# Kernel optimization log

Measured on AMD Instinct MI355X. Metric: run time of the kernel, lower is better.

Reference implementation:

```python
import jax, jax.numpy as jnp
import numpy as np

B, N, DIM, H = 2, 2048, 1024, 16
HD = DIM // H
SCALE = HD ** -0.5


def setup_inputs() -> dict:
    key = jax.random.key(0)
    ks = jax.random.split(key, 11)
    std = DIM ** -0.5
    inp = {
        'q': jax.random.normal(ks[0], (B, N, DIM), jnp.float32),
        'k': jax.random.normal(ks[1], (B, N, DIM), jnp.float32),
        'v': jax.random.normal(ks[2], (B, N, DIM), jnp.float32),
        # causal mask, broadcast over batch and heads; mask==0 -> masked out
        'mask': jnp.tril(jnp.ones((N, N), jnp.int32))[None, None],
        'Wq': jax.random.normal(ks[3], (DIM, DIM), jnp.float32) * std,
        'bq': jnp.zeros((DIM,), jnp.float32),
        'Wk': jax.random.normal(ks[4], (DIM, DIM), jnp.float32) * std,
        'bk': jnp.zeros((DIM,), jnp.float32),
        'Wv': jax.random.normal(ks[5], (DIM, DIM), jnp.float32) * std,
        'bv': jnp.zeros((DIM,), jnp.float32),
        'Wo': jax.random.normal(ks[6], (DIM, DIM), jnp.float32) * std,
        'bo': jnp.zeros((DIM,), jnp.float32),
    }
    return inp


def _split_heads(x):  # [b, n, dim] -> [b, h, n, c]
    b, n, _ = x.shape
    return x.reshape(b, n, H, HD).transpose(0, 2, 1, 3)


def reference(q, k, v, mask, Wq, bq, Wk, bk, Wv, bv, Wo, bo):
    qh = _split_heads(q @ Wq.T + bq)                      # [b,h,nq,c]
    kh = _split_heads(k @ Wk.T + bk)                      # [b,h,nk,c]
    vh = _split_heads(v @ Wv.T + bv)                      # [b,h,nk,c]
    attn = jnp.einsum('bhqc,bhkc->bhqk', qh, kh) * SCALE  # [b,h,nq,nk]
    attn = jnp.where(mask == 0, -jnp.inf, attn)
    attn = jax.nn.softmax(attn, axis=-1)
    out = jnp.einsum('bhqk,bhkc->bhqc', attn, vh)          # [b,h,nq,c]
    b, h, n, c = out.shape
    out = out.transpose(0, 2, 1, 3).reshape(b, n, h * c)   # [b,nq,dim]
    return out @ Wo.T + bo
```

## Files before the change

### kernel.cpp

```cpp
#include <hip/hip_runtime.h>

#define NN 2048
#define DIMD 1024
#define HH 16
#define HDD 64
#define SC2 0.1803368801111244f

typedef __attribute__((ext_vector_type(8))) short bf16x8;
typedef __attribute__((ext_vector_type(4))) float f32x4;
typedef __attribute__((ext_vector_type(4))) _Float16 f16x4;
typedef __attribute__((ext_vector_type(2))) __fp16 hf16x2;
typedef unsigned short ushort_t;
typedef unsigned int uint_t;

#define MFMA32(a, b, c) __builtin_amdgcn_mfma_f32_16x16x32_bf16((a), (b), (c), 0, 0, 0)
#define MFMA16H(a, b, c) __builtin_amdgcn_mfma_f32_16x16x16f16((a), (b), (c), 0, 0, 0)

__device__ __forceinline__ ushort_t f2bf(float f) {
    union { float f; uint_t u; } v; v.f = f;
    uint_t u = v.u;
    return (ushort_t)((u + 0x7FFFu + ((u >> 16) & 1u)) >> 16);
}
__device__ __forceinline__ void gl_lds16(const ushort_t* g, ushort_t* l) {
    __builtin_amdgcn_global_load_lds(
        (const __attribute__((address_space(1))) void*)g,
        (__attribute__((address_space(3))) void*)l, 16, 0, 0);
}

__global__ __launch_bounds__(256) void convert_k(
    const float* __restrict__ q, const float* __restrict__ k, const float* __restrict__ v,
    const float* __restrict__ wq, const float* __restrict__ wk,
    const float* __restrict__ wv, const float* __restrict__ wo,
    ushort_t* __restrict__ Abf, ushort_t* __restrict__ Wbf) {
    size_t gid = (size_t)blockIdx.x * 256 + threadIdx.x;
    size_t e = gid * 8;
    const float* src; ushort_t* dst;
    float sc = 1.f;
    if (e < 12582912) {
        int i = (int)(e >> 22);
        src = (i == 0 ? q : (i == 1 ? k : v)) + (e & 4194303);
        dst = Abf + e;
    } else {
        size_t e2 = e - 12582912;
        int i = (int)(e2 >> 20);
        src = (i == 0 ? wq : (i == 1 ? wk : (i == 2 ? wv : wo))) + (e2 & 1048575);
        dst = Wbf + e2;
        if (i == 0) sc = SC2;
    }
    float4 x = ((const float4*)src)[0], y = ((const float4*)src)[1];
    union { uint4 u; ushort_t s[8]; } pk;
    pk.s[0] = f2bf(x.x * sc); pk.s[1] = f2bf(x.y * sc); pk.s[2] = f2bf(x.z * sc); pk.s[3] = f2bf(x.w * sc);
    pk.s[4] = f2bf(y.x * sc); pk.s[5] = f2bf(y.y * sc); pk.s[6] = f2bf(y.z * sc); pk.s[7] = f2bf(y.w * sc);
    *(uint4*)dst = pk.u;
}

template<int MODE, int TM>
__global__ __launch_bounds__(256, TM == 128 ? 3 : 5) void gemm_k(
    const ushort_t* __restrict__ Abase, const ushort_t* __restrict__ Wbase,
    const float* __restrict__ b0p, const float* __restrict__ b1p, const float* __restrict__ b2p,
    ushort_t* __restrict__ d0, ushort_t* __restrict__ d1, ushort_t* __restrict__ d2,
    float* __restrict__ fout) {
    const int K = 1024;
    constexpr int MT = TM / 32;
    __shared__ ushort_t As[2][TM * 32];
    __shared__ ushort_t Bs[2][128 * 32];
    int z = (MODE == 0) ? blockIdx.z : 0;
    const ushort_t* A = Abase + (size_t)z * 4096 * 1024;
    const ushort_t* W = Wbase + (size_t)z * 1024 * 1024;
    const float* bias = (MODE == 0) ? (z == 0 ? b0p : (z == 1 ? b1p : b2p)) : b0p;
    int tid = threadIdx.x;
    int m0 = blockIdx.x * TM, n0 = blockIdx.y * 128;
    int lane = tid & 63, wave = tid >> 6;
    int quad = lane >> 4, l15 = lane & 15;
    int wm = (wave >> 1) * (TM / 2), wn = (wave & 1) * 64;

    f32x4 acc[MT][4];
    for (int i = 0; i < MT; i++)
        for (int j = 0; j < 4; j++)
            acc[i][j] = (f32x4){0.f, 0.f, 0.f, 0.f};

    int rA = tid >> 2, cA = tid & 3;
    int gA = cA ^ ((rA >> 1) & 3);

    auto stage = [&](int buf, int k0) {
        gl_lds16(A + (size_t)(m0 + rA) * K + k0 + gA * 8, &As[buf][tid * 8]);
        if (TM == 128)
            gl_lds16(A + (size_t)(m0 + rA + 64) * K + k0 + gA * 8, &As[buf][(tid + 256) * 8]);
        gl_lds16(W + (size_t)(n0 + rA) * K + k0 + gA * 8, &Bs[buf][tid * 8]);
        gl_lds16(W + (size_t)(n0 + rA + 64) * K + k0 + gA * 8, &Bs[buf][(tid + 256) * 8]);
    };
    stage(0, 0);

    int fc = (quad ^ ((l15 >> 1) & 3)) * 8;

    for (int it = 0; it < 32; it++) {
        int cur = it & 1;
        __syncthreads();
        if (it < 31) stage(1 - cur, (it + 1) * 32);
        bf16x8 a[MT], b[4];
        for (int mt = 0; mt < MT; mt++)
            a[mt] = *(const bf16x8*)&As[cur][(wm + mt * 16 + l15) * 32 + fc];
        for (int nt = 0; nt < 4; nt++)
            b[nt] = *(const bf16x8*)&Bs[cur][(wn + nt * 16 + l15) * 32 + fc];
        for (int mt = 0; mt < MT; mt++)
            for (int nt = 0; nt < 4; nt++)
                acc[mt][nt] = MFMA32(a[mt], b[nt], acc[mt][nt]);
    }
    if (MODE == 0 && z == 2) {
        for (int nt = 0; nt < 4; nt++) {
            int n = n0 + wn + nt * 16 + l15;
            float bv = bias[n];
            int h = n >> 6, c = n & 63;
            for (int mt = 0; mt < MT; mt++) {
                int mb = m0 + wm + mt * 16 + quad * 4;
                int b = mb >> 11, ns = mb & 2047;
                union { uint2 u2; _Float16 hh[4]; } pkv;
                pkv.hh[0] = (_Float16)(acc[mt][nt][0] + bv);
                pkv.hh[1] = (_Float16)(acc[mt][nt][1] + bv);
                pkv.hh[2] = (_Float16)(acc[mt][nt][2] + bv);
                pkv.hh[3] = (_Float16)(acc[mt][nt][3] + bv);
                *(uint2*)&d2[(((size_t)(b * HH + h)) * HDD + c) * NN + ns] = pkv.u2;
            }
        }
    } else {
        for (int nt = 0; nt < 4; nt++) {
            int n = n0 + wn + nt * 16 + l15;
            float bv = bias[n];
            if (MODE == 0 && z == 0) bv *= SC2;
            for (int mt = 0; mt < MT; mt++)
                for (int r = 0; r < 4; r++) {
                    int m = m0 + wm + mt * 16 + quad * 4 + r;
                    float val = acc[mt][nt][r] + bv;
                    if (MODE == 0) {
                        int b = m >> 11, ns = m & 2047;
                        int h = n >> 6, c = n & 63;
                        ushort_t* dst = (z == 0) ? d0 : d1;
                        dst[(((size_t)(b * HH + h)) * NN + ns) * HDD + c] = f2bf(val);
                    } else {
                        fout[(size_t)m * DIMD + n] = val;
                    }
                }
        }
    }
}

__global__ __launch_bounds__(256, 2) void attn9(const ushort_t* __restrict__ Qh,
                                                const ushort_t* __restrict__ Kh,
                                                const ushort_t* __restrict__ VtG,
                                                ushort_t* __restrict__ aout) {
    __shared__ ushort_t Kb[2][2][64 * 64];
    __shared__ ushort_t Vb[2][2][64 * 64];
    int tid = threadIdx.x, lane = tid & 63, w = tid >> 6;
    int quad = lane >> 4, l15 = lane & 15;
    int bh = blockIdx.y;
    int qa = blockIdx.x;
    int qc = 31 - qa;
    const ushort_t* Qp = Qh + (size_t)bh * NN * HDD;
    const ushort_t* Kp = Kh + (size_t)bh * NN * HDD;
    const ushort_t* Vp = VtG + (size_t)bh * HDD * NN;
    int ra = qa * 64 + w * 16;
    int rc = qc * 64 + w * 16;

    bf16x8 aqa[2], aqc[2];
    for (int kk = 0; kk < 2; kk++) {
        aqa[kk] = *(const bf16x8*)&Qp[(size_t)(ra + l15) * HDD + kk * 32 + quad * 8];
        aqc[kk] = *(const bf16x8*)&Qp[(size_t)(rc + l15) * HDD + kk * 32 + quad * 8];
    }
    asm volatile("" :: "v"(aqa[0]), "v"(aqa[1]), "v"(aqc[0]), "v"(aqc[1]));

    f32x4 oa[4], oc[4], ola, olc;
    for (int ct = 0; ct < 4; ct++) {
        oa[ct] = (f32x4){0.f, 0.f, 0.f, 0.f};
        oc[ct] = (f32x4){0.f, 0.f, 0.f, 0.f};
    }
    ola = (f32x4){0.f, 0.f, 0.f, 0.f};
    olc = (f32x4){0.f, 0.f, 0.f, 0.f};
    const f16x4 vone = {(_Float16)1.f, (_Float16)1.f, (_Float16)1.f, (_Float16)1.f};

    int sr0 = tid >> 3, scg = tid & 7;
    int ssc = scg ^ (sr0 & 7);
    int key = l15 & 7;
    int c0 = (quad ^ key) * 8;
    int c1 = ((4 + quad) ^ key) * 8;

    auto stageK = [&](int s, int kt) {
        for (int h = 0; h < 2; h++) {
            int kr = kt * 128 + h * 64;
            gl_lds16(Kp + (size_t)(kr + sr0) * HDD + ssc * 8,      &Kb[s][h][(0 * 256 + w * 64) * 8]);
            gl_lds16(Kp + (size_t)(kr + sr0 + 32) * HDD + ssc * 8, &Kb[s][h][(1 * 256 + w * 64) * 8]);
            gl_lds16(Vp + (size_t)sr0 * NN + kr + ssc * 8,         &Vb[s][h][(0 * 256 + w * 64) * 8]);
            gl_lds16(Vp + (size_t)(sr0 + 32) * NN + kr + ssc * 8,  &Vb[s][h][(1 * 256 + w * 64) * 8]);
        }
    };

    int kbmax = qc >> 1;
    int kam   = qa >> 1;
    stageK(0, 0);

    auto doHalf = [&](const bf16x8 (&aq)[2], f32x4 (&o)[4], f32x4& ol,
                      int rowb, const ushort_t* Kl, const ushort_t* Vl,
                      int kvb, bool diag) {
        bf16x8 kf0[4], kf1[4];
        for (int nt = 0; nt < 4; nt++) {
            kf0[nt] = *(const bf16x8*)&Kl[(nt * 16 + l15) * 64 + c0];
            kf1[nt] = *(const bf16x8*)&Kl[(nt * 16 + l15) * 64 + c1];
        }
        f32x4 s[4];
        __builtin_amdgcn_s_setprio(1);
        for (int nt = 0; nt < 4; nt++) {
            f32x4 z = (f32x4){0.f, 0.f, 0.f, 0.f};
            z = MFMA32(kf0[nt], aq[0], z);
            s[nt] = MFMA32(kf1[nt], aq[1], z);
        }
        __builtin_amdgcn_s_setprio(0);
        f16x4 ap[4];
        if (diag) {
            for (int nt = 0; nt < 4; nt++) {
                float pp[4];
                for (int r = 0; r < 4; r++) {
                    int kv = kvb + nt * 16 + quad * 4 + r;
                    pp[r] = (kv <= rowb + l15) ? __builtin_amdgcn_exp2f(s[nt][r]) : 0.f;
                }
                union { hf16x2 h2[2]; f16x4 h4; } u;
                u.h2[0] = __builtin_amdgcn_cvt_pkrtz(pp[0], pp[1]);
                u.h2[1] = __builtin_amdgcn_cvt_pkrtz(pp[2], pp[3]);
                ap[nt] = u.h4;
            }
        } else {
            for (int nt = 0; nt < 4; nt++) {
                union { hf16x2 h2[2]; f16x4 h4; } u;
                u.h2[0] = __builtin_amdgcn_cvt_pkrtz(__builtin_amdgcn_exp2f(s[nt][0]),
                                                     __builtin_amdgcn_exp2f(s[nt][1]));
                u.h2[1] = __builtin_amdgcn_cvt_pkrtz(__builtin_amdgcn_exp2f(s[nt][2]),
                                                     __builtin_amdgcn_exp2f(s[nt][3]));
                ap[nt] = u.h4;
            }
        }
        f16x4 vf[4][4];
        for (int ct = 0; ct < 4; ct++)
            for (int nt = 0; nt < 4; nt++)
                vf[ct][nt] = *(const f16x4*)&Vl[(ct * 16 + l15) * 64 +
                                ((2 * nt + (quad >> 1)) ^ key) * 8 + (quad & 1) * 4];
        __builtin_amdgcn_s_setprio(1);
        for (int nt = 0; nt < 4; nt++)
            ol = MFMA16H(ap[nt], vone, ol);
        for (int ct = 0; ct < 4; ct++)
            for (int nt = 0; nt < 4; nt++)
                o[ct] = MFMA16H(ap[nt], vf[ct][nt], o[ct]);
        __builtin_amdgcn_s_setprio(0);
    };

    int cur = 0;
    for (int kb2 = 0; kb2 <= kbmax; kb2++) {
        __syncthreads();
        if (kb2 < kbmax) stageK(cur ^ 1, kb2 + 1);
        bool dc = (kb2 == kbmax);
        for (int h = 0; h < 2; h++)
            doHalf(aqc, oc, olc, rc, &Kb[cur][h][0], &Vb[cur][h][0],
                   kb2 * 128 + h * 64, dc);
        if (kb2 <= kam) {
            bool da = (kb2 == kam);
            for (int h = 0; h < 2; h++)
                doHalf(aqa, oa, ola, ra, &Kb[cur][h][0], &Vb[cur][h][0],
                       kb2 * 128 + h * 64, da);
        }
        cur ^= 1;
    }

    int b = bh >> 4, h = bh & 15;
    for (int r = 0; r < 4; r++) {
        float ila = 1.f / ola[r];
        float ilc = 1.f / olc[r];
        for (int ct = 0; ct < 4; ct++) {
            int c = ct * 16 + l15;
            int qqa = ra + quad * 4 + r;
            int qqc = rc + quad * 4 + r;
            aout[((size_t)(b * NN + qqa)) * DIMD + h * HDD + c] = f2bf(oa[ct][r] * ila);
            aout[((size_t)(b * NN + qqc)) * DIMD + h * HDD + c] = f2bf(oc[ct][r] * ilc);
        }
    }
}

extern "C" void kernel_launch(void* const* d_in, const int* in_sizes, int n_in,
                              void* d_out, int out_size, void* d_ws, size_t ws_size,
                              hipStream_t stream) {
    const float* q  = (const float*)d_in[0];
    const float* k  = (const float*)d_in[1];
    const float* v  = (const float*)d_in[2];
    const float* Wq = (const float*)d_in[4];
    const float* bq = (const float*)d_in[5];
    const float* Wk = (const float*)d_in[6];
    const float* bk = (const float*)d_in[7];
    const float* Wv = (const float*)d_in[8];
    const float* bv = (const float*)d_in[9];
    const float* Wo = (const float*)d_in[10];
    const float* bo = (const float*)d_in[11];
    float* out = (float*)d_out;

    char* ws = (char*)d_ws;
    ushort_t* Abf  = (ushort_t*)(ws);
    ushort_t* Wbf  = (ushort_t*)(ws + (24ull << 20));
    ushort_t* Qh   = (ushort_t*)(ws + (32ull << 20));
    ushort_t* Kh   = (ushort_t*)(ws + (40ull << 20));
    ushort_t* VtG  = (ushort_t*)(ws + (48ull << 20));
    ushort_t* AObf = (ushort_t*)(ws + (56ull << 20));

    hipLaunchKernelGGL(convert_k, dim3(8192), dim3(256), 0, stream,
                       q, k, v, Wq, Wk, Wv, Wo, Abf, Wbf);
    hipLaunchKernelGGL((gemm_k<0, 128>), dim3(32, 8, 3), dim3(256), 0, stream,
                       Abf, Wbf, bq, bk, bv, Qh, Kh, VtG, (float*)nullptr);
    hipLaunchKernelGGL(attn9, dim3(16, 32), dim3(256), 0, stream, Qh, Kh, VtG, AObf);
    hipLaunchKernelGGL((gemm_k<1, 64>), dim3(64, 8, 1), dim3(256), 0, stream,
                       AObf, Wbf + 3ull * 1024 * 1024, bo, nullptr, nullptr,
                       nullptr, nullptr, nullptr, out);
}
```

Before: 221.0 us.

## Fuse fp32-to-bf16 activation conversion into the QKV projection GEMM

The separate conversion of q, k and v to bf16 is removed. A new QKV GEMM kernel reads the fp32 activations directly into registers, converts them with packed bf16 convert instructions, and writes them into swizzled LDS, while the weights are still staged through global_load_lds. This removes a full write and re-read of the 24MB bf16 activation copy. In exchange the GEMM reads twice as many bytes for A and does the conversion work inside its main loop, which may lengthen each loop iteration.

```diff
diff --git a/kernel.cpp b/kernel.cpp
--- a/kernel.cpp
+++ b/kernel.cpp
@@ -27,31 +27,121 @@
         (__attribute__((address_space(3))) void*)l, 16, 0, 0);
 }
 
-__global__ __launch_bounds__(256) void convert_k(
-    const float* __restrict__ q, const float* __restrict__ k, const float* __restrict__ v,
+__global__ __launch_bounds__(256) void convert_w(
     const float* __restrict__ wq, const float* __restrict__ wk,
     const float* __restrict__ wv, const float* __restrict__ wo,
-    ushort_t* __restrict__ Abf, ushort_t* __restrict__ Wbf) {
-    size_t gid = (size_t)blockIdx.x * 256 + threadIdx.x;
-    size_t e = gid * 8;
-    const float* src; ushort_t* dst;
-    float sc = 1.f;
-    if (e < 12582912) {
-        int i = (int)(e >> 22);
-        src = (i == 0 ? q : (i == 1 ? k : v)) + (e & 4194303);
-        dst = Abf + e;
-    } else {
-        size_t e2 = e - 12582912;
-        int i = (int)(e2 >> 20);
-        src = (i == 0 ? wq : (i == 1 ? wk : (i == 2 ? wv : wo))) + (e2 & 1048575);
-        dst = Wbf + e2;
-        if (i == 0) sc = SC2;
-    }
+    ushort_t* __restrict__ Wbf) {
+    size_t e2 = ((size_t)blockIdx.x * 256 + threadIdx.x) * 8;
+    int i = (int)(e2 >> 20);
+    const float* src = (i == 0 ? wq : (i == 1 ? wk : (i == 2 ? wv : wo))) + (e2 & 1048575);
+    float sc = (i == 0) ? SC2 : 1.f;
     float4 x = ((const float4*)src)[0], y = ((const float4*)src)[1];
     union { uint4 u; ushort_t s[8]; } pk;
     pk.s[0] = f2bf(x.x * sc); pk.s[1] = f2bf(x.y * sc); pk.s[2] = f2bf(x.z * sc); pk.s[3] = f2bf(x.w * sc);
     pk.s[4] = f2bf(y.x * sc); pk.s[5] = f2bf(y.y * sc); pk.s[6] = f2bf(y.z * sc); pk.s[7] = f2bf(y.w * sc);
-    *(uint4*)dst = pk.u;
+    *(uint4*)(Wbf + e2) = pk.u;
+}
+
+__global__ __launch_bounds__(256, 3) void gemm_qkv(
+    const float* __restrict__ qf, const float* __restrict__ kf,
+    const float* __restrict__ vf,
+    const ushort_t* __restrict__ Wbase,
+    const float* __restrict__ b0p, const float* __restrict__ b1p, const float* __restrict__ b2p,
+    ushort_t* __restrict__ d0, ushort_t* __restrict__ d1, ushort_t* __restrict__ d2) {
+    const int K = 1024;
+    __shared__ ushort_t As[2][128 * 32];
+    __shared__ ushort_t Bs[2][128 * 32];
+    int z = blockIdx.z;
+    const float* A32 = (z == 0 ? qf : (z == 1 ? kf : vf));
+    const ushort_t* W = Wbase + (size_t)z * 1024 * 1024;
+    const float* bias = (z == 0 ? b0p : (z == 1 ? b1p : b2p));
+    int tid = threadIdx.x;
+    int m0 = blockIdx.x * 128, n0 = blockIdx.y * 128;
+    int lane = tid & 63, wave = tid >> 6;
+    int quad = lane >> 4, l15 = lane & 15;
+    int wm = (wave >> 1) * 64, wn = (wave & 1) * 64;
+
+    f32x4 acc[4][4];
+    for (int i = 0; i < 4; i++)
+        for (int j = 0; j < 4; j++)
+            acc[i][j] = (f32x4){0.f, 0.f, 0.f, 0.f};
+
+    int rA = tid >> 2, cA = tid & 3;
+    int gA = cA ^ ((rA >> 1) & 3);
+
+    float4 ar[4];
+    auto issueA = [&](int k0) {
+        const float* p0 = A32 + (size_t)(m0 + rA) * K + k0 + gA * 8;
+        const float* p1 = A32 + (size_t)(m0 + rA + 64) * K + k0 + gA * 8;
+        ar[0] = ((const float4*)p0)[0]; ar[1] = ((const float4*)p0)[1];
+        ar[2] = ((const float4*)p1)[0]; ar[3] = ((const float4*)p1)[1];
+    };
+    auto cvt8 = [&](const float4& x, const float4& y) {
+        uint4 r;
+        asm("v_cvt_pk_bf16_f32 %0, %1, %2" : "=v"(r.x) : "v"(x.x), "v"(x.y));
+        asm("v_cvt_pk_bf16_f32 %0, %1, %2" : "=v"(r.y) : "v"(x.z), "v"(x.w));
+        asm("v_cvt_pk_bf16_f32 %0, %1, %2" : "=v"(r.z) : "v"(y.x), "v"(y.y));
+        asm("v_cvt_pk_bf16_f32 %0, %1, %2" : "=v"(r.w) : "v"(y.z), "v"(y.w));
+        return r;
+    };
+    auto writeA = [&](int buf) {
+        *(uint4*)&As[buf][tid * 8] = cvt8(ar[0], ar[1]);
+        *(uint4*)&As[buf][(tid + 256) * 8] = cvt8(ar[2], ar[3]);
+    };
+    auto stageW = [&](int buf, int k0) {
+        gl_lds16(W + (size_t)(n0 + rA) * K + k0 + gA * 8, &Bs[buf][tid * 8]);
+        gl_lds16(W + (size_t)(n0 + rA + 64) * K + k0 + gA * 8, &Bs[buf][(tid + 256) * 8]);
+    };
+    issueA(0); stageW(0, 0); writeA(0);
+
+    int fc = (quad ^ ((l15 >> 1) & 3)) * 8;
+
+    for (int it = 0; it < 32; it++) {
+        int cur = it & 1;
+        __syncthreads();
+        if (it < 31) { issueA((it + 1) * 32); stageW(1 - cur, (it + 1) * 32); }
+        bf16x8 a[4], b[4];
+        for (int mt = 0; mt < 4; mt++)
+            a[mt] = *(const bf16x8*)&As[cur][(wm + mt * 16 + l15) * 32 + fc];
+        for (int nt = 0; nt < 4; nt++)
+            b[nt] = *(const bf16x8*)&Bs[cur][(wn + nt * 16 + l15) * 32 + fc];
+        for (int mt = 0; mt < 4; mt++)
+            for (int nt = 0; nt < 4; nt++)
+                acc[mt][nt] = MFMA32(a[mt], b[nt], acc[mt][nt]);
+        if (it < 31) writeA(1 - cur);
+    }
+    if (z == 2) {
+        for (int nt = 0; nt < 4; nt++) {
+            int n = n0 + wn + nt * 16 + l15;
+            float bv = bias[n];
+            int h = n >> 6, c = n & 63;
+            for (int mt = 0; mt < 4; mt++) {
+                int mb = m0 + wm + mt * 16 + quad * 4;
+                int b = mb >> 11, ns = mb & 2047;
+                union { uint2 u2; _Float16 hh[4]; } pkv;
+                pkv.hh[0] = (_Float16)(acc[mt][nt][0] + bv);
+                pkv.hh[1] = (_Float16)(acc[mt][nt][1] + bv);
+                pkv.hh[2] = (_Float16)(acc[mt][nt][2] + bv);
+                pkv.hh[3] = (_Float16)(acc[mt][nt][3] + bv);
+                *(uint2*)&d2[(((size_t)(b * HH + h)) * HDD + c) * NN + ns] = pkv.u2;
+            }
+        }
+    } else {
+        for (int nt = 0; nt < 4; nt++) {
+            int n = n0 + wn + nt * 16 + l15;
+            float bv = bias[n];
+            if (z == 0) bv *= SC2;
+            for (int mt = 0; mt < 4; mt++)
+                for (int r = 0; r < 4; r++) {
+                    int m = m0 + wm + mt * 16 + quad * 4 + r;
+                    float val = acc[mt][nt][r] + bv;
+                    int b = m >> 11, ns = m & 2047;
+                    int h = n >> 6, c = n & 63;
+                    ushort_t* dst = (z == 0) ? d0 : d1;
+                    dst[(((size_t)(b * HH + h)) * NN + ns) * HDD + c] = f2bf(val);
+                }
+        }
+    }
 }
 
 template<int MODE, int TM>
@@ -298,17 +388,16 @@
     float* out = (float*)d_out;
 
     char* ws = (char*)d_ws;
-    ushort_t* Abf  = (ushort_t*)(ws);
-    ushort_t* Wbf  = (ushort_t*)(ws + (24ull << 20));
-    ushort_t* Qh   = (ushort_t*)(ws + (32ull << 20));
-    ushort_t* Kh   = (ushort_t*)(ws + (40ull << 20));
-    ushort_t* VtG  = (ushort_t*)(ws + (48ull << 20));
-    ushort_t* AObf = (ushort_t*)(ws + (56ull << 20));
-
-    hipLaunchKernelGGL(convert_k, dim3(8192), dim3(256), 0, stream,
-                       q, k, v, Wq, Wk, Wv, Wo, Abf, Wbf);
-    hipLaunchKernelGGL((gemm_k<0, 128>), dim3(32, 8, 3), dim3(256), 0, stream,
-                       Abf, Wbf, bq, bk, bv, Qh, Kh, VtG, (float*)nullptr);
+    ushort_t* Wbf  = (ushort_t*)(ws);
+    ushort_t* Qh   = (ushort_t*)(ws + (8ull << 20));
+    ushort_t* Kh   = (ushort_t*)(ws + (16ull << 20));
+    ushort_t* VtG  = (ushort_t*)(ws + (24ull << 20));
+    ushort_t* AObf = (ushort_t*)(ws + (32ull << 20));
+
+    hipLaunchKernelGGL(convert_w, dim3(2048), dim3(256), 0, stream,
+                       Wq, Wk, Wv, Wo, Wbf);
+    hipLaunchKernelGGL(gemm_qkv, dim3(32, 8, 3), dim3(256), 0, stream,
+                       q, k, v, Wbf, bq, bk, bv, Qh, Kh, VtG);
     hipLaunchKernelGGL(attn9, dim3(16, 32), dim3(256), 0, stream, Qh, Kh, VtG, AObf);
     hipLaunchKernelGGL((gemm_k<1, 64>), dim3(64, 8, 1), dim3(256), 0, stream,
                        AObf, Wbf + 3ull * 1024 * 1024, bo, nullptr, nullptr,
```

Result: slower. 226.8 us (+2.6%).
